# Kernel tuning notes

Measured on AMD Instinct MI355X. Metric: run time of the kernel, lower is better.

## Reference

```python
import jax, jax.numpy as jnp
import numpy as np

B, T, E, H, M = 1, 2048, 1536, 16, 3
KVH = 8
NREP = H // KVH
HD = E // H // M  # 32
EPS = 1e-5


def setup_inputs() -> dict:
    key = jax.random.key(0)
    ks = jax.random.split(key, 6)
    x = jax.random.normal(ks[0], (B, T, E), jnp.float32)
    # true rotary tables: freqs = pos * 10000^{-2i/d}, shape [T, HD//2]
    inv_freq = 1.0 / (10000.0 ** (np.arange(0, HD, 2, dtype=np.float64) / HD))
    ang = np.outer(np.arange(T, dtype=np.float64), inv_freq)
    cos = jnp.asarray(np.cos(ang), jnp.float32)
    sin = jnp.asarray(np.sin(ang), jnp.float32)
    s = 0.02
    q_w = s * jax.random.normal(ks[1], (M, E // M, E), jnp.float32)
    k_w = s * jax.random.normal(ks[2], (M, E // M // NREP, E), jnp.float32)
    v_w = s * jax.random.normal(ks[3], (E // NREP, E), jnp.float32)
    out_w = s * jax.random.normal(ks[4], (E, E), jnp.float32)
    raw_map_weights = jnp.array([0.1, -0.1, 0.1], jnp.float32)
    weight_scale = jnp.ones((1,), jnp.float32)
    subln_w = jnp.ones((M * HD,), jnp.float32)
    return dict(x=x, cos=cos, sin=sin, q_w=q_w, k_w=k_w, v_w=v_w,
                out_w=out_w, raw_map_weights=raw_map_weights,
                weight_scale=weight_scale, subln_w=subln_w)


def _rope_interleaved(t, cos, sin):
    # t: [..., seq, heads, hd]; cos/sin: [seq, hd//2]
    x1 = t[..., 0::2]
    x2 = t[..., 1::2]
    c = cos[:, None, :]
    s = sin[:, None, :]
    o1 = x1 * c - x2 * s
    o2 = x1 * s + x2 * c
    return jnp.stack([o1, o2], axis=-1).reshape(t.shape)


def reference(x, cos, sin, q_w, k_w, v_w, out_w, raw_map_weights, weight_scale, subln_w):
    b, t, e = x.shape
    m = q_w.shape[0]
    hd = 2 * cos.shape[-1]
    h = q_w.shape[1] // hd
    kvh = k_w.shape[1] // hd
    nrep = h // kvh
    scaling = hd ** -0.5

    map_w = jnp.tanh(raw_map_weights) * weight_scale  # [M]

    # per-map Q/K projections, all maps at once
    q = jnp.einsum('bte,mfe->mbtf', x, q_w).reshape(m, b, t, h, hd)
    k = jnp.einsum('bte,mfe->mbtf', x, k_w).reshape(m, b, t, kvh, hd)
    q = _rope_interleaved(q, cos, sin) * scaling
    k = _rope_interleaved(k, cos, sin)
    q = q.transpose(0, 1, 3, 2, 4)                      # [m,b,h,t,hd]
    k = jnp.repeat(k.transpose(0, 1, 3, 2, 4), nrep, axis=2)  # [m,b,h,t,hd]

    v = jnp.einsum('bte,fe->btf', x, v_w).reshape(b, t, kvh, m * hd)
    v = jnp.repeat(v.transpose(0, 2, 1, 3), nrep, axis=1)  # [b,h,t,m*hd]

    causal = jnp.where(jnp.triu(jnp.ones((t, t), bool), 1),
                       jnp.float32(-jnp.inf), jnp.float32(0.0))

    scores = jnp.einsum('mbhtd,mbhsd->mbhts', q, k)
    scores = jnp.nan_to_num(scores) + causal
    attn_w = jax.nn.softmax(scores.astype(jnp.float32), axis=-1).astype(x.dtype)
    combined = jnp.einsum('m,mbhts->bhts', map_w, attn_w)

    attn = jnp.einsum('bhts,bhsf->bhtf', combined, v)  # [b,h,t,m*hd]
    # RMSNorm over last dim
    var = jnp.mean(jnp.square(attn.astype(jnp.float32)), axis=-1, keepdims=True)
    attn = (attn * jax.lax.rsqrt(var + EPS)).astype(attn.dtype) * subln_w

    attn = attn.transpose(0, 2, 1, 3).reshape(b, t, h * m * hd)
    return jnp.einsum('bte,fe->btf', attn, out_w)
```

## Files before the change

### kernel.cpp

```cpp
#include <hip/hip_runtime.h>
#include <hip/hip_bf16.h>
#include <math.h>

#define T_DIM 2048
#define E_DIM 1536
#define K_DIM 1536

typedef unsigned short u16;
typedef unsigned int u32;
typedef __attribute__((ext_vector_type(8))) short bf16x8;
typedef __attribute__((ext_vector_type(4))) float f32x4;

__device__ __forceinline__ u16 f2bf(float x) {
    unsigned u = __float_as_uint(x);
    return (u16)((u + 0x7fffu + ((u >> 16) & 1u)) >> 16);
}

#define GLOAD16(gsrc, ldst)                                                              \
    __builtin_amdgcn_global_load_lds((const __attribute__((address_space(1))) u32*)(gsrc), \
                                     (__attribute__((address_space(3))) u32*)(ldst), 16, 0, 0)

__global__ __launch_bounds__(256) void cvt_bf16_5(const float* __restrict__ s0, u16* __restrict__ d0,
                                                  const float* __restrict__ s1, u16* __restrict__ d1,
                                                  const float* __restrict__ s2, u16* __restrict__ d2,
                                                  const float* __restrict__ s3, u16* __restrict__ d3,
                                                  const float* __restrict__ s4, u16* __restrict__ d4) {
    int i = blockIdx.x * 256 + threadIdx.x;
    const float* s;
    u16* d;
    int off;
    if (i < 786432)       { s = s0; d = d0; off = i; }
    else if (i < 1376256) { s = s1; d = d1; off = i - 786432; }
    else if (i < 1671168) { s = s2; d = d2; off = i - 1376256; }
    else if (i < 1966080) { s = s3; d = d3; off = i - 1671168; }
    else                  { s = s4; d = d4; off = i - 1966080; }
    float4 v = ((const float4*)s)[off];
    ((ushort4*)d)[off] = make_ushort4(f2bf(v.x), f2bf(v.y), f2bf(v.z), f2bf(v.w));
}

__global__ __launch_bounds__(256) void gemm_qkv_fused(const u16* __restrict__ A,
                                                      const u16* __restrict__ W,
                                                      const float* __restrict__ cosb,
                                                      const float* __restrict__ sinb,
                                                      u16* __restrict__ qb16,
                                                      u16* __restrict__ kpack,
                                                      u16* __restrict__ vpack,
                                                      float qscale) {
    const int K = K_DIM;
    __shared__ __align__(16) u16 As[128 * 64];
    __shared__ __align__(16) u16 Bs[128 * 64];
    const int tid = threadIdx.x;
    const int lane = tid & 63;
    const int wv = tid >> 6;
    const int wr = wv >> 1;
    const int wc = wv & 1;
    const int cl = lane & 15;
    const int g = lane >> 4;
    const int bm = blockIdx.y * 128;
    const int bn = blockIdx.x * 128;

    const char* Ab = (const char*)A;
    const char* Wb = (const char*)W;

    size_t a_src[4], b_src[4];
    int dst[4];
#pragma unroll
    for (int is = 0; is < 4; ++is) {
        int b = is * 4096 + tid * 16;
        int row = b >> 7;
        int wi = b & 127;
        dst[is] = b;
        a_src[is] = (size_t)(bm + row) * (K * 2) + (wi ^ ((row & 7) << 4));
        b_src[is] = (size_t)(bn + row) * (K * 2) + (wi ^ ((row & 7) << 4));
    }

    f32x4 acc[4][4];
#pragma unroll
    for (int mi = 0; mi < 4; ++mi)
#pragma unroll
        for (int ni = 0; ni < 4; ++ni) acc[mi][ni] = (f32x4){0.f, 0.f, 0.f, 0.f};

    for (int k0b = 0; k0b < K * 2; k0b += 128) {
#pragma unroll
        for (int is = 0; is < 4; ++is)
            GLOAD16(Ab + a_src[is] + k0b, (char*)As + dst[is]);
#pragma unroll
        for (int is = 0; is < 4; ++is)
            GLOAD16(Wb + b_src[is] + k0b, (char*)Bs + dst[is]);
        __syncthreads();
#pragma unroll
        for (int kk = 0; kk < 2; ++kk) {
            const int co = (kk * 64 + g * 16) ^ ((cl & 7) << 4);
            bf16x8 af[4], bfr[4];
#pragma unroll
            for (int mi = 0; mi < 4; ++mi)
                af[mi] = *(const bf16x8*)((const char*)As + (wr * 64 + mi * 16 + cl) * 128 + co);
#pragma unroll
            for (int ni = 0; ni < 4; ++ni)
                bfr[ni] = *(const bf16x8*)((const char*)Bs + (wc * 64 + ni * 16 + cl) * 128 + co);
#pragma unroll
            for (int mi = 0; mi < 4; ++mi)
#pragma unroll
                for (int ni = 0; ni < 4; ++ni)
                    acc[mi][ni] = __builtin_amdgcn_mfma_f32_16x16x32_bf16(af[mi], bfr[ni], acc[mi][ni], 0, 0, 0);
        }
        __syncthreads();
    }

    if (bn < 1536) {
#pragma unroll
        for (int mi = 0; mi < 4; ++mi)
#pragma unroll
            for (int ni = 0; ni < 4; ++ni)
#pragma unroll
                for (int r = 0; r < 4; ++r) {
                    int trow = bm + wr * 64 + mi * 16 + 4 * g + r;
                    int c = bn + wc * 64 + ni * 16 + cl;
                    float v = acc[mi][ni][r];
                    float pv = __shfl_xor(v, 1, 64);
                    int i = (c & 31) >> 1;
                    float cs = cosb[trow * 16 + i];
                    float sn = sinb[trow * 16 + i];
                    float o = v * cs + ((c & 1) ? pv * sn : -pv * sn);
                    qb16[(size_t)trow * E_DIM + c] = f2bf(o * qscale);
                }
    } else if (bn < 2304) {
#pragma unroll
        for (int mi = 0; mi < 4; ++mi)
#pragma unroll
            for (int ni = 0; ni < 4; ++ni)
#pragma unroll
                for (int r = 0; r < 4; ++r) {
                    int trow = bm + wr * 64 + mi * 16 + 4 * g + r;
                    int c = bn + wc * 64 + ni * 16 + cl;
                    float v = acc[mi][ni][r];
                    float pv = __shfl_xor(v, 1, 64);
                    int i = (c & 31) >> 1;
                    float cs = cosb[trow * 16 + i];
                    float sn = sinb[trow * 16 + i];
                    float o = v * cs + ((c & 1) ? pv * sn : -pv * sn);
                    int ck = c - 1536;
                    int m = ck >> 8;
                    int rem = ck & 255;
                    int kvhh = rem >> 5;
                    int d = rem & 31;
                    int cch = trow >> 5, st2 = (trow >> 4) & 1, colk = trow & 15;
                    size_t dstb = ((((size_t)(kvhh * 64 + cch) * 3 + m) * 2 + st2) * 16 + colk) * 32 + d;
                    kpack[dstb] = f2bf(o);
                }
    } else {
#pragma unroll
        for (int mi = 0; mi < 4; ++mi)
#pragma unroll
            for (int ni = 0; ni < 4; ++ni)
#pragma unroll
                for (int r = 0; r < 4; ++r) {
                    int trow = bm + wr * 64 + mi * 16 + 4 * g + r;
                    int c = bn + wc * 64 + ni * 16 + cl;
                    int fq = c - 2304;
                    int kvhh = fq / 96;
                    int f = fq - kvhh * 96;
                    size_t dstb = ((size_t)(kvhh * 64 + (trow >> 5)) * 96 + f) * 32 + (trow & 31);
                    vpack[dstb] = f2bf(acc[mi][ni][r]);
                }
    }
}

__global__ __launch_bounds__(256) void gemm_mfma_out(const u16* __restrict__ A,
                                                     const u16* __restrict__ W,
                                                     float* __restrict__ Cp,
                                                     int K, int ldC) {
    __shared__ __align__(16) u16 As[128 * 64];
    __shared__ __align__(16) u16 Bs[64 * 64];
    const int tid = threadIdx.x;
    const int lane = tid & 63;
    const int wv = tid >> 6;
    const int wr = wv >> 1;
    const int wc = wv & 1;
    const int cl = lane & 15;
    const int g = lane >> 4;
    const int bm = blockIdx.y * 128;
    const int bn = blockIdx.x * 64;

    const char* Ab = (const char*)A;
    const char* Wb = (const char*)W;

    size_t a_src[4];
    int a_dst[4];
#pragma unroll
    for (int is = 0; is < 4; ++is) {
        int b = is * 4096 + wv * 1024 + lane * 16;
        int row = b >> 7;
        int wi = b & 127;
        a_src[is] = (size_t)(bm + row) * (K * 2) + (wi ^ ((row & 7) << 4));
        a_dst[is] = b;
    }
    size_t b_src[2];
    int b_dst[2];
#pragma unroll
    for (int is = 0; is < 2; ++is) {
        int b = is * 4096 + wv * 1024 + lane * 16;
        int row = b >> 7;
        int wi = b & 127;
        b_src[is] = (size_t)(bn + row) * (K * 2) + (wi ^ ((row & 7) << 4));
        b_dst[is] = b;
    }

    f32x4 acc[4][2];
#pragma unroll
    for (int mi = 0; mi < 4; ++mi)
#pragma unroll
        for (int ni = 0; ni < 2; ++ni) acc[mi][ni] = (f32x4){0.f, 0.f, 0.f, 0.f};

    for (int k0b = 0; k0b < K * 2; k0b += 128) {
#pragma unroll
        for (int is = 0; is < 4; ++is)
            GLOAD16(Ab + a_src[is] + k0b, (char*)As + a_dst[is]);
#pragma unroll
        for (int is = 0; is < 2; ++is)
            GLOAD16(Wb + b_src[is] + k0b, (char*)Bs + b_dst[is]);
        __syncthreads();
#pragma unroll
        for (int kk = 0; kk < 2; ++kk) {
            const int co = (kk * 64 + g * 16) ^ ((cl & 7) << 4);
            bf16x8 af[4], bfr[2];
#pragma unroll
            for (int mi = 0; mi < 4; ++mi)
                af[mi] = *(const bf16x8*)((const char*)As + (wr * 64 + mi * 16 + cl) * 128 + co);
#pragma unroll
            for (int ni = 0; ni < 2; ++ni)
                bfr[ni] = *(const bf16x8*)((const char*)Bs + (wc * 32 + ni * 16 + cl) * 128 + co);
#pragma unroll
            for (int mi = 0; mi < 4; ++mi)
#pragma unroll
                for (int ni = 0; ni < 2; ++ni)
                    acc[mi][ni] = __builtin_amdgcn_mfma_f32_16x16x32_bf16(af[mi], bfr[ni], acc[mi][ni], 0, 0, 0);
        }
        __syncthreads();
    }

#pragma unroll
    for (int mi = 0; mi < 4; ++mi)
#pragma unroll
        for (int ni = 0; ni < 2; ++ni)
#pragma unroll
            for (int r = 0; r < 4; ++r) {
                size_t row = bm + wr * 64 + mi * 16 + 4 * g + r;
                size_t col = bn + wc * 32 + ni * 16 + cl;
                Cp[row * ldC + col] = acc[mi][ni][r];
            }
}

__global__ __launch_bounds__(256) void attn_fused(const u16* __restrict__ qb,
                                                  const u16* __restrict__ kpack,
                                                  const u16* __restrict__ vpack,
                                                  const float* __restrict__ raw_map,
                                                  const float* __restrict__ wscale,
                                                  const float* __restrict__ subln,
                                                  u16* __restrict__ outb) {
    __shared__ __align__(16) char smem[12288];
    const int tid = threadIdx.x;
    const int lane = tid & 63;
    const int wv = tid >> 6;
    const int col = lane & 15;
    const int g = lane >> 4;
    const int lid = blockIdx.x;
    const int kvh = lid & 7;
    const int rest = lid >> 3;
    const int h = kvh * 2 + (rest & 1);
    const int p = rest >> 1;

    u16 (*plds)[2][16][40] = (u16(*)[2][16][40])smem;
    float (*red2)[48] = (float(*)[48])smem;
    float (*red1)[3][2][16] = (float(*)[3][2][16])smem;

    float mw[3];
    {
        float wsc = wscale[0];
#pragma unroll
        for (int m = 0; m < 3; ++m) mw[m] = tanhf(raw_map[m]) * wsc;
    }
    const int laneoff = col * 32 + 8 * g;

    for (int half = 0; half < 2; ++half) {
        const int qt = half ? p : (63 - p);
        const int qbase = qt * 32;
        const int nfull = qt;

        bf16x8 qfrag[3][2];
#pragma unroll
        for (int m = 0; m < 3; ++m)
#pragma unroll
            for (int q2 = 0; q2 < 2; ++q2)
                qfrag[m][q2] = *(const bf16x8*)(qb + (size_t)(qbase + 16 * q2 + col) * E_DIM + m * 512 + h * 32 + 8 * g);

        float lsum[3][2] = {{0.f, 0.f}, {0.f, 0.f}, {0.f, 0.f}};
        {
            const u16* kt = kpack + (size_t)(kvh * 64 + wv) * 3072;
            for (int c = wv; c < nfull; c += 4) {
                bf16x8 kf[6];
#pragma unroll
                for (int u = 0; u < 6; ++u) kf[u] = *(const bf16x8*)(kt + laneoff + u * 512);
                kt += 4 * 3072;
                __builtin_amdgcn_s_setprio(1);
#pragma unroll
                for (int m = 0; m < 3; ++m)
#pragma unroll
                    for (int st = 0; st < 2; ++st)
#pragma unroll
                        for (int q2 = 0; q2 < 2; ++q2) {
                            f32x4 sv = __builtin_amdgcn_mfma_f32_16x16x32_bf16(
                                kf[m * 2 + st], qfrag[m][q2], (f32x4){0.f, 0.f, 0.f, 0.f}, 0, 0, 0);
                            lsum[m][q2] += (__builtin_amdgcn_exp2f(sv[0]) + __builtin_amdgcn_exp2f(sv[1])) +
                                           (__builtin_amdgcn_exp2f(sv[2]) + __builtin_amdgcn_exp2f(sv[3]));
                        }
                __builtin_amdgcn_s_setprio(0);
            }
            if ((nfull & 3) == wv) {
                const u16* ktm = kpack + (size_t)(kvh * 64 + nfull) * 3072 + laneoff;
                bf16x8 kf[6];
#pragma unroll
                for (int u = 0; u < 6; ++u) kf[u] = *(const bf16x8*)(ktm + u * 512);
#pragma unroll
                for (int m = 0; m < 3; ++m) {
                    {
                        f32x4 sv = __builtin_amdgcn_mfma_f32_16x16x32_bf16(
                            kf[m * 2 + 0], qfrag[m][0], (f32x4){0.f, 0.f, 0.f, 0.f}, 0, 0, 0);
#pragma unroll
                        for (int r = 0; r < 4; ++r) {
                            float x = (4 * g + r > col) ? -1e30f : sv[r];
                            lsum[m][0] += __builtin_amdgcn_exp2f(x);
                        }
                    }
                    {
                        f32x4 sv = __builtin_amdgcn_mfma_f32_16x16x32_bf16(
                            kf[m * 2 + 0], qfrag[m][1], (f32x4){0.f, 0.f, 0.f, 0.f}, 0, 0, 0);
                        lsum[m][1] += (__builtin_amdgcn_exp2f(sv[0]) + __builtin_amdgcn_exp2f(sv[1])) +
                                      (__builtin_amdgcn_exp2f(sv[2]) + __builtin_amdgcn_exp2f(sv[3]));
                    }
                    {
                        f32x4 sv = __builtin_amdgcn_mfma_f32_16x16x32_bf16(
                            kf[m * 2 + 1], qfrag[m][1], (f32x4){0.f, 0.f, 0.f, 0.f}, 0, 0, 0);
#pragma unroll
                        for (int r = 0; r < 4; ++r) {
                            float x = (4 * g + r > col) ? -1e30f : sv[r];
                            lsum[m][1] += __builtin_amdgcn_exp2f(x);
                        }
                    }
                }
            }
        }
#pragma unroll
        for (int m = 0; m < 3; ++m)
#pragma unroll
            for (int q2 = 0; q2 < 2; ++q2) {
                lsum[m][q2] += __shfl_xor(lsum[m][q2], 16, 64);
                lsum[m][q2] += __shfl_xor(lsum[m][q2], 32, 64);
            }
        if (g == 0) {
#pragma unroll
            for (int m = 0; m < 3; ++m)
#pragma unroll
                for (int q2 = 0; q2 < 2; ++q2) red1[wv][m][q2][col] = lsum[m][q2];
        }
        __syncthreads();
        float fac[3][2];
#pragma unroll
        for (int m = 0; m < 3; ++m)
#pragma unroll
            for (int q2 = 0; q2 < 2; ++q2)
                fac[m][q2] = mw[m] / (red1[0][m][q2][col] + red1[1][m][q2][col] +
                                      red1[2][m][q2][col] + red1[3][m][q2][col]);
        __syncthreads();

        f32x4 oacc[2][6];
#pragma unroll
        for (int q2 = 0; q2 < 2; ++q2)
#pragma unroll
            for (int ft = 0; ft < 6; ++ft) oacc[q2][ft] = (f32x4){0.f, 0.f, 0.f, 0.f};

        {
            const u16* kt = kpack + (size_t)(kvh * 64 + wv) * 3072;
            const u16* vt = vpack + (size_t)(kvh * 64 + wv) * 3072;
            for (int c = wv; c < nfull; c += 4) {
                bf16x8 kf[6], vf[6];
#pragma unroll
                for (int u = 0; u < 6; ++u) kf[u] = *(const bf16x8*)(kt + laneoff + u * 512);
#pragma unroll
                for (int u = 0; u < 6; ++u) vf[u] = *(const bf16x8*)(vt + laneoff + u * 512);
                kt += 4 * 3072;
                vt += 4 * 3072;

                __builtin_amdgcn_s_setprio(1);
#pragma unroll
                for (int q2 = 0; q2 < 2; ++q2)
#pragma unroll
                    for (int st = 0; st < 2; ++st) {
                        float pp[4] = {0.f, 0.f, 0.f, 0.f};
#pragma unroll
                        for (int m = 0; m < 3; ++m) {
                            f32x4 sv = __builtin_amdgcn_mfma_f32_16x16x32_bf16(
                                kf[m * 2 + st], qfrag[m][q2], (f32x4){0.f, 0.f, 0.f, 0.f}, 0, 0, 0);
#pragma unroll
                            for (int r = 0; r < 4; ++r)
                                pp[r] += fac[m][q2] * __builtin_amdgcn_exp2f(sv[r]);
                        }
                        __hip_bfloat162 b01 = __float22bfloat162_rn(make_float2(pp[0], pp[1]));
                        __hip_bfloat162 b23 = __float22bfloat162_rn(make_float2(pp[2], pp[3]));
                        uint2 w;
                        w.x = *(u32*)&b01;
                        w.y = *(u32*)&b23;
                        *(uint2*)&plds[wv][q2][col][st * 16 + 4 * g] = w;
                    }
#pragma unroll
                for (int q2 = 0; q2 < 2; ++q2) {
                    bf16x8 pf = *(const bf16x8*)&plds[wv][q2][col][8 * g];
#pragma unroll
                    for (int ft = 0; ft < 6; ++ft)
                        oacc[q2][ft] = __builtin_amdgcn_mfma_f32_16x16x32_bf16(pf, vf[ft], oacc[q2][ft], 0, 0, 0);
                }
                __builtin_amdgcn_s_setprio(0);
            }

            if ((nfull & 3) == wv) {
                const u16* ktm = kpack + (size_t)(kvh * 64 + nfull) * 3072 + laneoff;
                const u16* vtm = vpack + (size_t)(kvh * 64 + nfull) * 3072 + laneoff;
                bf16x8 kf[6], vf[6];
#pragma unroll
                for (int u = 0; u < 6; ++u) kf[u] = *(const bf16x8*)(ktm + u * 512);
#pragma unroll
                for (int u = 0; u < 6; ++u) vf[u] = *(const bf16x8*)(vtm + u * 512);

                {
                    float pp[4] = {0.f, 0.f, 0.f, 0.f};
#pragma unroll
                    for (int m = 0; m < 3; ++m) {
                        f32x4 sv = __builtin_amdgcn_mfma_f32_16x16x32_bf16(
                            kf[m * 2 + 0], qfrag[m][0], (f32x4){0.f, 0.f, 0.f, 0.f}, 0, 0, 0);
#pragma unroll
                        for (int r = 0; r < 4; ++r) {
                            float x = (4 * g + r > col) ? -1e30f : sv[r];
                            pp[r] += fac[m][0] * __builtin_amdgcn_exp2f(x);
                        }
                    }
                    __hip_bfloat162 b01 = __float22bfloat162_rn(make_float2(pp[0], pp[1]));
                    __hip_bfloat162 b23 = __float22bfloat162_rn(make_float2(pp[2], pp[3]));
                    uint2 w;
                    w.x = *(u32*)&b01;
                    w.y = *(u32*)&b23;
                    *(uint2*)&plds[wv][0][col][4 * g] = w;
                    uint2 z = make_uint2(0u, 0u);
                    *(uint2*)&plds[wv][0][col][16 + 4 * g] = z;
                }
                {
                    float p0[4] = {0.f, 0.f, 0.f, 0.f};
                    float p1[4] = {0.f, 0.f, 0.f, 0.f};
#pragma unroll
                    for (int m = 0; m < 3; ++m) {
                        f32x4 sv0 = __builtin_amdgcn_mfma_f32_16x16x32_bf16(
                            kf[m * 2 + 0], qfrag[m][1], (f32x4){0.f, 0.f, 0.f, 0.f}, 0, 0, 0);
                        f32x4 sv1 = __builtin_amdgcn_mfma_f32_16x16x32_bf16(
                            kf[m * 2 + 1], qfrag[m][1], (f32x4){0.f, 0.f, 0.f, 0.f}, 0, 0, 0);
#pragma unroll
                        for (int r = 0; r < 4; ++r) {
                            p0[r] += fac[m][1] * __builtin_amdgcn_exp2f(sv0[r]);
                            float x = (4 * g + r > col) ? -1e30f : sv1[r];
                            p1[r] += fac[m][1] * __builtin_amdgcn_exp2f(x);
                        }
                    }
                    __hip_bfloat162 a01 = __float22bfloat162_rn(make_float2(p0[0], p0[1]));
                    __hip_bfloat162 a23 = __float22bfloat162_rn(make_float2(p0[2], p0[3]));
                    uint2 w0;
                    w0.x = *(u32*)&a01;
                    w0.y = *(u32*)&a23;
                    *(uint2*)&plds[wv][1][col][4 * g] = w0;
                    __hip_bfloat162 b01 = __float22bfloat162_rn(make_float2(p1[0], p1[1]));
                    __hip_bfloat162 b23 = __float22bfloat162_rn(make_float2(p1[2], p1[3]));
                    uint2 w1;
                    w1.x = *(u32*)&b01;
                    w1.y = *(u32*)&b23;
                    *(uint2*)&plds[wv][1][col][16 + 4 * g] = w1;
                }
#pragma unroll
                for (int q2 = 0; q2 < 2; ++q2) {
                    bf16x8 pf = *(const bf16x8*)&plds[wv][q2][col][8 * g];
#pragma unroll
                    for (int ft = 0; ft < 6; ++ft)
                        oacc[q2][ft] = __builtin_amdgcn_mfma_f32_16x16x32_bf16(pf, vf[ft], oacc[q2][ft], 0, 0, 0);
                }
            }
        }

        __syncthreads();
#pragma unroll
        for (int src = 1; src < 4; ++src) {
            if (wv == src) {
                float4* rp = (float4*)red2[lane];
#pragma unroll
                for (int q2 = 0; q2 < 2; ++q2)
#pragma unroll
                    for (int ft = 0; ft < 6; ++ft)
                        rp[q2 * 6 + ft] = make_float4(oacc[q2][ft][0], oacc[q2][ft][1],
                                                      oacc[q2][ft][2], oacc[q2][ft][3]);
            }
            __syncthreads();
            if (wv == 0) {
                const float4* rp = (const float4*)red2[lane];
#pragma unroll
                for (int q2 = 0; q2 < 2; ++q2)
#pragma unroll
                    for (int ft = 0; ft < 6; ++ft) {
                        float4 a = rp[q2 * 6 + ft];
                        oacc[q2][ft][0] += a.x; oacc[q2][ft][1] += a.y;
                        oacc[q2][ft][2] += a.z; oacc[q2][ft][3] += a.w;
                    }
            }
            __syncthreads();
        }

        if (wv == 0) {
            float ss[2][4] = {{0.f, 0.f, 0.f, 0.f}, {0.f, 0.f, 0.f, 0.f}};
#pragma unroll
            for (int q2 = 0; q2 < 2; ++q2)
#pragma unroll
                for (int ft = 0; ft < 6; ++ft)
#pragma unroll
                    for (int r = 0; r < 4; ++r) ss[q2][r] += oacc[q2][ft][r] * oacc[q2][ft][r];
#pragma unroll
            for (int q2 = 0; q2 < 2; ++q2)
#pragma unroll
                for (int r = 0; r < 4; ++r) {
                    ss[q2][r] += __shfl_xor(ss[q2][r], 1, 64);
                    ss[q2][r] += __shfl_xor(ss[q2][r], 2, 64);
                    ss[q2][r] += __shfl_xor(ss[q2][r], 4, 64);
                    ss[q2][r] += __shfl_xor(ss[q2][r], 8, 64);
                    ss[q2][r] = rsqrtf(ss[q2][r] * (1.f / 96.f) + 1e-5f);
                }
#pragma unroll
            for (int ft = 0; ft < 6; ++ft) {
                float sl = subln[ft * 16 + col];
#pragma unroll
                for (int q2 = 0; q2 < 2; ++q2)
#pragma unroll
                    for (int r = 0; r < 4; ++r) {
                        int trow = qbase + 16 * q2 + 4 * g + r;
                        outb[(size_t)trow * E_DIM + h * 96 + ft * 16 + col] =
                            f2bf(oacc[q2][ft][r] * ss[q2][r] * sl);
                    }
            }
        }
        __syncthreads();
    }
}

extern "C" void kernel_launch(void* const* d_in, const int* in_sizes, int n_in,
                              void* d_out, int out_size, void* d_ws, size_t ws_size,
                              hipStream_t stream) {
    const float* x       = (const float*)d_in[0];
    const float* cosb    = (const float*)d_in[1];
    const float* sinb    = (const float*)d_in[2];
    const float* q_w     = (const float*)d_in[3];
    const float* k_w     = (const float*)d_in[4];
    const float* v_w     = (const float*)d_in[5];
    const float* out_w   = (const float*)d_in[6];
    const float* raw_map = (const float*)d_in[7];
    const float* wscale  = (const float*)d_in[8];
    const float* subln   = (const float*)d_in[9];
    float* out = (float*)d_out;

    char* ws = (char*)d_ws;
    u16* xb16   = (u16*)(ws);
    u16* wqkv16 = (u16*)(ws + 6291456);
    u16* qb16   = (u16*)(ws + 15728640);
    u16* kpack  = (u16*)(ws + 22020096);
    u16* vpack  = (u16*)(ws + 25190400);
    u16* wout16 = (u16*)(ws + 28360704);
    u16* ab16   = xb16;

    cvt_bf16_5<<<9984, 256, 0, stream>>>(x, xb16,
                                         q_w, wqkv16,
                                         k_w, wqkv16 + 2359296,
                                         v_w, wqkv16 + 3538944,
                                         out_w, wout16);

    const float qscale = 0.17677669529663687f * 1.4426950408889634f;
    gemm_qkv_fused<<<dim3(3072 / 128, T_DIM / 128), 256, 0, stream>>>(
        xb16, wqkv16, cosb, sinb, qb16, kpack, vpack, qscale);

    attn_fused<<<512, 256, 0, stream>>>(qb16, kpack, vpack, raw_map, wscale, subln, ab16);

    gemm_mfma_out<<<dim3(E_DIM / 64, T_DIM / 128), 256, 0, stream>>>(ab16, wout16, out, K_DIM, E_DIM);
}
```

Measured before the change: 127.4 us.

## Use eight waves per attention block with a tree reduction of partial outputs

Doubles the attention kernel's block size from four to eight waves, so each block splits its causal key tiles across eight waves instead of four. The cross-wave reduction of the partial output accumulators becomes a three-level tree over a larger shared-memory buffer, replacing the sequential one-wave-at-a-time reduction. The aim is to raise per-block parallelism and latency hiding on a grid of only 512 blocks. The cost is more shared memory per block and added reduction and synchronisation overhead, and the launch-bounds change may limit registers per thread.

Result: slower. 311.0 us (+144.2%).

```diff
diff --git a/kernel.cpp b/kernel.cpp
--- a/kernel.cpp
+++ b/kernel.cpp
@@ -251,14 +251,14 @@
             }
 }
 
-__global__ __launch_bounds__(256) void attn_fused(const u16* __restrict__ qb,
-                                                  const u16* __restrict__ kpack,
-                                                  const u16* __restrict__ vpack,
-                                                  const float* __restrict__ raw_map,
-                                                  const float* __restrict__ wscale,
-                                                  const float* __restrict__ subln,
-                                                  u16* __restrict__ outb) {
-    __shared__ __align__(16) char smem[12288];
+__global__ __launch_bounds__(512, 4) void attn_fused(const u16* __restrict__ qb,
+                                                     const u16* __restrict__ kpack,
+                                                     const u16* __restrict__ vpack,
+                                                     const float* __restrict__ raw_map,
+                                                     const float* __restrict__ wscale,
+                                                     const float* __restrict__ subln,
+                                                     u16* __restrict__ outb) {
+    __shared__ __align__(16) char smem[49152];
     const int tid = threadIdx.x;
     const int lane = tid & 63;
     const int wv = tid >> 6;
@@ -271,8 +271,8 @@
     const int p = rest >> 1;
 
     u16 (*plds)[2][16][40] = (u16(*)[2][16][40])smem;
-    float (*red2)[48] = (float(*)[48])smem;
     float (*red1)[3][2][16] = (float(*)[3][2][16])smem;
+    float* redA = (float*)smem;
 
     float mw[3];
     {
@@ -297,11 +297,11 @@
         float lsum[3][2] = {{0.f, 0.f}, {0.f, 0.f}, {0.f, 0.f}};
         {
             const u16* kt = kpack + (size_t)(kvh * 64 + wv) * 3072;
-            for (int c = wv; c < nfull; c += 4) {
+            for (int c = wv; c < nfull; c += 8) {
                 bf16x8 kf[6];
 #pragma unroll
                 for (int u = 0; u < 6; ++u) kf[u] = *(const bf16x8*)(kt + laneoff + u * 512);
-                kt += 4 * 3072;
+                kt += 8 * 3072;
                 __builtin_amdgcn_s_setprio(1);
 #pragma unroll
                 for (int m = 0; m < 3; ++m)
@@ -316,7 +316,7 @@
                         }
                 __builtin_amdgcn_s_setprio(0);
             }
-            if ((nfull & 3) == wv) {
+            if ((nfull & 7) == wv) {
                 const u16* ktm = kpack + (size_t)(kvh * 64 + nfull) * 3072 + laneoff;
                 bf16x8 kf[6];
 #pragma unroll
@@ -368,9 +368,12 @@
 #pragma unroll
         for (int m = 0; m < 3; ++m)
 #pragma unroll
-            for (int q2 = 0; q2 < 2; ++q2)
-                fac[m][q2] = mw[m] / (red1[0][m][q2][col] + red1[1][m][q2][col] +
-                                      red1[2][m][q2][col] + red1[3][m][q2][col]);
+            for (int q2 = 0; q2 < 2; ++q2) {
+                float tot = 0.f;
+#pragma unroll
+                for (int w8 = 0; w8 < 8; ++w8) tot += red1[w8][m][q2][col];
+                fac[m][q2] = mw[m] / tot;
+            }
         __syncthreads();
 
         f32x4 oacc[2][6];
@@ -382,14 +385,14 @@
         {
             const u16* kt = kpack + (size_t)(kvh * 64 + wv) * 3072;
             const u16* vt = vpack + (size_t)(kvh * 64 + wv) * 3072;
-            for (int c = wv; c < nfull; c += 4) {
+            for (int c = wv; c < nfull; c += 8) {
                 bf16x8 kf[6], vf[6];
 #pragma unroll
                 for (int u = 0; u < 6; ++u) kf[u] = *(const bf16x8*)(kt + laneoff + u * 512);
 #pragma unroll
                 for (int u = 0; u < 6; ++u) vf[u] = *(const bf16x8*)(vt + laneoff + u * 512);
-                kt += 4 * 3072;
-                vt += 4 * 3072;
+                kt += 8 * 3072;
+                vt += 8 * 3072;
 
                 __builtin_amdgcn_s_setprio(1);
 #pragma unroll
@@ -422,7 +425,7 @@
                 __builtin_amdgcn_s_setprio(0);
             }
 
-            if ((nfull & 3) == wv) {
+            if ((nfull & 7) == wv) {
                 const u16* ktm = kpack + (size_t)(kvh * 64 + nfull) * 3072 + laneoff;
                 const u16* vtm = vpack + (size_t)(kvh * 64 + nfull) * 3072 + laneoff;
                 bf16x8 kf[6], vf[6];
@@ -492,33 +495,71 @@
         }
 
         __syncthreads();
-#pragma unroll
-        for (int src = 1; src < 4; ++src) {
-            if (wv == src) {
-                float4* rp = (float4*)red2[lane];
-#pragma unroll
-                for (int q2 = 0; q2 < 2; ++q2)
-#pragma unroll
-                    for (int ft = 0; ft < 6; ++ft)
-                        rp[q2 * 6 + ft] = make_float4(oacc[q2][ft][0], oacc[q2][ft][1],
-                                                      oacc[q2][ft][2], oacc[q2][ft][3]);
-            }
-            __syncthreads();
-            if (wv == 0) {
-                const float4* rp = (const float4*)red2[lane];
-#pragma unroll
-                for (int q2 = 0; q2 < 2; ++q2)
-#pragma unroll
-                    for (int ft = 0; ft < 6; ++ft) {
-                        float4 a = rp[q2 * 6 + ft];
-                        oacc[q2][ft][0] += a.x; oacc[q2][ft][1] += a.y;
-                        oacc[q2][ft][2] += a.z; oacc[q2][ft][3] += a.w;
-                    }
-            }
-            __syncthreads();
-        }
-
+        if (wv >= 4) {
+            float4* rp = (float4*)(redA + ((size_t)(wv - 4) * 64 + lane) * 48);
+#pragma unroll
+            for (int q2 = 0; q2 < 2; ++q2)
+#pragma unroll
+                for (int ft = 0; ft < 6; ++ft)
+                    rp[q2 * 6 + ft] = make_float4(oacc[q2][ft][0], oacc[q2][ft][1],
+                                                  oacc[q2][ft][2], oacc[q2][ft][3]);
+        }
+        __syncthreads();
+        if (wv < 4) {
+            const float4* rp = (const float4*)(redA + ((size_t)wv * 64 + lane) * 48);
+#pragma unroll
+            for (int q2 = 0; q2 < 2; ++q2)
+#pragma unroll
+                for (int ft = 0; ft < 6; ++ft) {
+                    float4 a = rp[q2 * 6 + ft];
+                    oacc[q2][ft][0] += a.x; oacc[q2][ft][1] += a.y;
+                    oacc[q2][ft][2] += a.z; oacc[q2][ft][3] += a.w;
+                }
+        }
+        __syncthreads();
+        if (wv == 2 || wv == 3) {
+            float4* rp = (float4*)(redA + ((size_t)(wv - 2) * 64 + lane) * 48);
+#pragma unroll
+            for (int q2 = 0; q2 < 2; ++q2)
+#pragma unroll
+                for (int ft = 0; ft < 6; ++ft)
+                    rp[q2 * 6 + ft] = make_float4(oacc[q2][ft][0], oacc[q2][ft][1],
+                                                  oacc[q2][ft][2], oacc[q2][ft][3]);
+        }
+        __syncthreads();
+        if (wv < 2) {
+            const float4* rp = (const float4*)(redA + ((size_t)wv * 64 + lane) * 48);
+#pragma unroll
+            for (int q2 = 0; q2 < 2; ++q2)
+#pragma unroll
+                for (int ft = 0; ft < 6; ++ft) {
+                    float4 a = rp[q2 * 6 + ft];
+                    oacc[q2][ft][0] += a.x; oacc[q2][ft][1] += a.y;
+                    oacc[q2][ft][2] += a.z; oacc[q2][ft][3] += a.w;
+                }
+        }
+        __syncthreads();
+        if (wv == 1) {
+            float4* rp = (float4*)(redA + (size_t)lane * 48);
+#pragma unroll
+            for (int q2 = 0; q2 < 2; ++q2)
+#pragma unroll
+                for (int ft = 0; ft < 6; ++ft)
+                    rp[q2 * 6 + ft] = make_float4(oacc[q2][ft][0], oacc[q2][ft][1],
+                                                  oacc[q2][ft][2], oacc[q2][ft][3]);
+        }
+        __syncthreads();
         if (wv == 0) {
+            const float4* rp = (const float4*)(redA + (size_t)lane * 48);
+#pragma unroll
+            for (int q2 = 0; q2 < 2; ++q2)
+#pragma unroll
+                for (int ft = 0; ft < 6; ++ft) {
+                    float4 a = rp[q2 * 6 + ft];
+                    oacc[q2][ft][0] += a.x; oacc[q2][ft][1] += a.y;
+                    oacc[q2][ft][2] += a.z; oacc[q2][ft][3] += a.w;
+                }
+
             float ss[2][4] = {{0.f, 0.f, 0.f, 0.f}, {0.f, 0.f, 0.f, 0.f}};
 #pragma unroll
             for (int q2 = 0; q2 < 2; ++q2)
@@ -587,7 +628,7 @@
     gemm_qkv_fused<<<dim3(3072 / 128, T_DIM / 128), 256, 0, stream>>>(
         xb16, wqkv16, cosb, sinb, qb16, kpack, vpack, qscale);
 
-    attn_fused<<<512, 256, 0, stream>>>(qb16, kpack, vpack, raw_map, wscale, subln, ab16);
+    attn_fused<<<512, 512, 0, stream>>>(qb16, kpack, vpack, raw_map, wscale, subln, ab16);
 
     gemm_mfma_out<<<dim3(E_DIM / 64, T_DIM / 128), 256, 0, stream>>>(ab16, wout16, out, K_DIM, E_DIM);
 }
```

## Fuse softmax sum and PV into one pass with post-normalization per map

Applied to the files above, without the earlier changes.

Replaces the two-pass attention kernel with a single-pass kernel. It accumulates unnormalized exp(QK)·V separately per map, then scales each map's partial output by map_weight/row_sum before summing across maps. This removes the separate row-sum pass, which recomputed every QK MFMA and exp. The work is also regrouped: 6 waves per block (3 maps × 2 key-strided waves), one 32-row query tile per block with heavy tiles launched first, instead of each block pairing a light and a heavy tile. The cost is a larger LDS reduction across 6 waves and extra bf16 rounding of unnormalized probabilities.

After: 133.7 us. +5.0%, slower.

```diff
diff --git a/kernel.cpp b/kernel.cpp
--- a/kernel.cpp
+++ b/kernel.cpp
@@ -251,305 +251,245 @@
             }
 }
 
-__global__ __launch_bounds__(256) void attn_fused(const u16* __restrict__ qb,
-                                                  const u16* __restrict__ kpack,
-                                                  const u16* __restrict__ vpack,
-                                                  const float* __restrict__ raw_map,
-                                                  const float* __restrict__ wscale,
-                                                  const float* __restrict__ subln,
-                                                  u16* __restrict__ outb) {
-    __shared__ __align__(16) char smem[12288];
+__global__ __launch_bounds__(384) void attn_one(const u16* __restrict__ qb,
+                                                const u16* __restrict__ kpack,
+                                                const u16* __restrict__ vpack,
+                                                const float* __restrict__ raw_map,
+                                                const float* __restrict__ wscale,
+                                                const float* __restrict__ subln,
+                                                u16* __restrict__ outb) {
+    __shared__ __align__(16) char smem[36864];
     const int tid = threadIdx.x;
     const int lane = tid & 63;
     const int wv = tid >> 6;
+    const int m = wv >> 1;
+    const int ks = wv & 1;
     const int col = lane & 15;
     const int g = lane >> 4;
-    const int lid = blockIdx.x;
+    const int lid = blockIdx.y * 64 + blockIdx.x;
     const int kvh = lid & 7;
     const int rest = lid >> 3;
     const int h = kvh * 2 + (rest & 1);
-    const int p = rest >> 1;
-
-    u16 (*plds)[2][16][40] = (u16(*)[2][16][40])smem;
-    float (*red2)[48] = (float(*)[48])smem;
-    float (*red1)[3][2][16] = (float(*)[3][2][16])smem;
-
-    float mw[3];
+    const int qt = 63 - (rest >> 1);
+    const int qbase = qt * 32;
+    const int nfull = qt;
+
+    u16 (*plds)[2][16][48] = (u16(*)[2][16][48])smem;
+    float (*red1)[2][16] = (float(*)[2][16])smem;
+
+    bf16x8 qfrag[2];
+#pragma unroll
+    for (int q2 = 0; q2 < 2; ++q2)
+        qfrag[q2] = *(const bf16x8*)(qb + (size_t)(qbase + 16 * q2 + col) * E_DIM + m * 512 + h * 32 + 8 * g);
+
+    f32x4 oacc[2][6];
+#pragma unroll
+    for (int q2 = 0; q2 < 2; ++q2)
+#pragma unroll
+        for (int ft = 0; ft < 6; ++ft) oacc[q2][ft] = (f32x4){0.f, 0.f, 0.f, 0.f};
+    float lsum[2] = {0.f, 0.f};
+
+    const int laneoff = col * 32 + 8 * g;
+    const u16* kt = kpack + ((size_t)(kvh * 64 + ks) * 3 + m) * 1024 + laneoff;
+    const u16* vt = vpack + (size_t)(kvh * 64 + ks) * 3072 + laneoff;
+
+    for (int c = ks; c < nfull; c += 2) {
+        bf16x8 kf0 = *(const bf16x8*)(kt);
+        bf16x8 kf1 = *(const bf16x8*)(kt + 512);
+        bf16x8 vf[6];
+#pragma unroll
+        for (int u = 0; u < 6; ++u) vf[u] = *(const bf16x8*)(vt + u * 512);
+        kt += 2 * 3072;
+        vt += 2 * 3072;
+
+        __builtin_amdgcn_s_setprio(1);
+#pragma unroll
+        for (int q2 = 0; q2 < 2; ++q2) {
+            f32x4 sv0 = __builtin_amdgcn_mfma_f32_16x16x32_bf16(kf0, qfrag[q2], (f32x4){0.f, 0.f, 0.f, 0.f}, 0, 0, 0);
+            f32x4 sv1 = __builtin_amdgcn_mfma_f32_16x16x32_bf16(kf1, qfrag[q2], (f32x4){0.f, 0.f, 0.f, 0.f}, 0, 0, 0);
+            float p0 = __builtin_amdgcn_exp2f(sv0[0]);
+            float p1 = __builtin_amdgcn_exp2f(sv0[1]);
+            float p2 = __builtin_amdgcn_exp2f(sv0[2]);
+            float p3 = __builtin_amdgcn_exp2f(sv0[3]);
+            float p4 = __builtin_amdgcn_exp2f(sv1[0]);
+            float p5 = __builtin_amdgcn_exp2f(sv1[1]);
+            float p6 = __builtin_amdgcn_exp2f(sv1[2]);
+            float p7 = __builtin_amdgcn_exp2f(sv1[3]);
+            lsum[q2] += ((p0 + p1) + (p2 + p3)) + ((p4 + p5) + (p6 + p7));
+            __hip_bfloat162 a01 = __float22bfloat162_rn(make_float2(p0, p1));
+            __hip_bfloat162 a23 = __float22bfloat162_rn(make_float2(p2, p3));
+            __hip_bfloat162 b01 = __float22bfloat162_rn(make_float2(p4, p5));
+            __hip_bfloat162 b23 = __float22bfloat162_rn(make_float2(p6, p7));
+            uint2 w0, w1;
+            w0.x = *(u32*)&a01; w0.y = *(u32*)&a23;
+            w1.x = *(u32*)&b01; w1.y = *(u32*)&b23;
+            *(uint2*)&plds[wv][q2][col][4 * g] = w0;
+            *(uint2*)&plds[wv][q2][col][16 + 4 * g] = w1;
+        }
+#pragma unroll
+        for (int q2 = 0; q2 < 2; ++q2) {
+            bf16x8 pf = *(const bf16x8*)&plds[wv][q2][col][8 * g];
+#pragma unroll
+            for (int ft = 0; ft < 6; ++ft)
+                oacc[q2][ft] = __builtin_amdgcn_mfma_f32_16x16x32_bf16(pf, vf[ft], oacc[q2][ft], 0, 0, 0);
+        }
+        __builtin_amdgcn_s_setprio(0);
+    }
+
+    if ((nfull & 1) == ks) {
+        const u16* ktm = kpack + ((size_t)(kvh * 64 + nfull) * 3 + m) * 1024 + laneoff;
+        const u16* vtm = vpack + (size_t)(kvh * 64 + nfull) * 3072 + laneoff;
+        bf16x8 kf0 = *(const bf16x8*)(ktm);
+        bf16x8 kf1 = *(const bf16x8*)(ktm + 512);
+        bf16x8 vf[6];
+#pragma unroll
+        for (int u = 0; u < 6; ++u) vf[u] = *(const bf16x8*)(vtm + u * 512);
+
+        {
+            f32x4 sv = __builtin_amdgcn_mfma_f32_16x16x32_bf16(kf0, qfrag[0], (f32x4){0.f, 0.f, 0.f, 0.f}, 0, 0, 0);
+            float p[4];
+#pragma unroll
+            for (int r = 0; r < 4; ++r) {
+                float x = (4 * g + r > col) ? -1e30f : sv[r];
+                p[r] = __builtin_amdgcn_exp2f(x);
+                lsum[0] += p[r];
+            }
+            __hip_bfloat162 a01 = __float22bfloat162_rn(make_float2(p[0], p[1]));
+            __hip_bfloat162 a23 = __float22bfloat162_rn(make_float2(p[2], p[3]));
+            uint2 w0;
+            w0.x = *(u32*)&a01; w0.y = *(u32*)&a23;
+            *(uint2*)&plds[wv][0][col][4 * g] = w0;
+            uint2 z = make_uint2(0u, 0u);
+            *(uint2*)&plds[wv][0][col][16 + 4 * g] = z;
+        }
+        {
+            f32x4 sv0 = __builtin_amdgcn_mfma_f32_16x16x32_bf16(kf0, qfrag[1], (f32x4){0.f, 0.f, 0.f, 0.f}, 0, 0, 0);
+            f32x4 sv1 = __builtin_amdgcn_mfma_f32_16x16x32_bf16(kf1, qfrag[1], (f32x4){0.f, 0.f, 0.f, 0.f}, 0, 0, 0);
+            float p0[4], p1[4];
+#pragma unroll
+            for (int r = 0; r < 4; ++r) {
+                p0[r] = __builtin_amdgcn_exp2f(sv0[r]);
+                float x = (4 * g + r > col) ? -1e30f : sv1[r];
+                p1[r] = __builtin_amdgcn_exp2f(x);
+                lsum[1] += p0[r] + p1[r];
+            }
+            __hip_bfloat162 a01 = __float22bfloat162_rn(make_float2(p0[0], p0[1]));
+            __hip_bfloat162 a23 = __float22bfloat162_rn(make_float2(p0[2], p0[3]));
+            __hip_bfloat162 b01 = __float22bfloat162_rn(make_float2(p1[0], p1[1]));
+            __hip_bfloat162 b23 = __float22bfloat162_rn(make_float2(p1[2], p1[3]));
+            uint2 w0, w1;
+            w0.x = *(u32*)&a01; w0.y = *(u32*)&a23;
+            w1.x = *(u32*)&b01; w1.y = *(u32*)&b23;
+            *(uint2*)&plds[wv][1][col][4 * g] = w0;
+            *(uint2*)&plds[wv][1][col][16 + 4 * g] = w1;
+        }
+#pragma unroll
+        for (int q2 = 0; q2 < 2; ++q2) {
+            bf16x8 pf = *(const bf16x8*)&plds[wv][q2][col][8 * g];
+#pragma unroll
+            for (int ft = 0; ft < 6; ++ft)
+                oacc[q2][ft] = __builtin_amdgcn_mfma_f32_16x16x32_bf16(pf, vf[ft], oacc[q2][ft], 0, 0, 0);
+        }
+    }
+
+#pragma unroll
+    for (int q2 = 0; q2 < 2; ++q2) {
+        lsum[q2] += __shfl_xor(lsum[q2], 16, 64);
+        lsum[q2] += __shfl_xor(lsum[q2], 32, 64);
+    }
+    __syncthreads();
+    if (g == 0) {
+#pragma unroll
+        for (int q2 = 0; q2 < 2; ++q2) red1[wv][q2][col] = lsum[q2];
+    }
+    __syncthreads();
+
     {
-        float wsc = wscale[0];
-#pragma unroll
-        for (int m = 0; m < 3; ++m) mw[m] = tanhf(raw_map[m]) * wsc;
-    }
-    const int laneoff = col * 32 + 8 * g;
-
-    for (int half = 0; half < 2; ++half) {
-        const int qt = half ? p : (63 - p);
-        const int qbase = qt * 32;
-        const int nfull = qt;
-
-        bf16x8 qfrag[3][2];
-#pragma unroll
-        for (int m = 0; m < 3; ++m)
-#pragma unroll
-            for (int q2 = 0; q2 < 2; ++q2)
-                qfrag[m][q2] = *(const bf16x8*)(qb + (size_t)(qbase + 16 * q2 + col) * E_DIM + m * 512 + h * 32 + 8 * g);
-
-        float lsum[3][2] = {{0.f, 0.f}, {0.f, 0.f}, {0.f, 0.f}};
-        {
-            const u16* kt = kpack + (size_t)(kvh * 64 + wv) * 3072;
-            for (int c = wv; c < nfull; c += 4) {
-                bf16x8 kf[6];
-#pragma unroll
-                for (int u = 0; u < 6; ++u) kf[u] = *(const bf16x8*)(kt + laneoff + u * 512);
-                kt += 4 * 3072;
-                __builtin_amdgcn_s_setprio(1);
-#pragma unroll
-                for (int m = 0; m < 3; ++m)
-#pragma unroll
-                    for (int st = 0; st < 2; ++st)
-#pragma unroll
-                        for (int q2 = 0; q2 < 2; ++q2) {
-                            f32x4 sv = __builtin_amdgcn_mfma_f32_16x16x32_bf16(
-                                kf[m * 2 + st], qfrag[m][q2], (f32x4){0.f, 0.f, 0.f, 0.f}, 0, 0, 0);
-                            lsum[m][q2] += (__builtin_amdgcn_exp2f(sv[0]) + __builtin_amdgcn_exp2f(sv[1])) +
-                                           (__builtin_amdgcn_exp2f(sv[2]) + __builtin_amdgcn_exp2f(sv[3]));
-                        }
-                __builtin_amdgcn_s_setprio(0);
-            }
-            if ((nfull & 3) == wv) {
-                const u16* ktm = kpack + (size_t)(kvh * 64 + nfull) * 3072 + laneoff;
-                bf16x8 kf[6];
-#pragma unroll
-                for (int u = 0; u < 6; ++u) kf[u] = *(const bf16x8*)(ktm + u * 512);
-#pragma unroll
-                for (int m = 0; m < 3; ++m) {
-                    {
-                        f32x4 sv = __builtin_amdgcn_mfma_f32_16x16x32_bf16(
-                            kf[m * 2 + 0], qfrag[m][0], (f32x4){0.f, 0.f, 0.f, 0.f}, 0, 0, 0);
-#pragma unroll
-                        for (int r = 0; r < 4; ++r) {
-                            float x = (4 * g + r > col) ? -1e30f : sv[r];
-                            lsum[m][0] += __builtin_amdgcn_exp2f(x);
-                        }
-                    }
-                    {
-                        f32x4 sv = __builtin_amdgcn_mfma_f32_16x16x32_bf16(
-                            kf[m * 2 + 0], qfrag[m][1], (f32x4){0.f, 0.f, 0.f, 0.f}, 0, 0, 0);
-                        lsum[m][1] += (__builtin_amdgcn_exp2f(sv[0]) + __builtin_amdgcn_exp2f(sv[1])) +
-                                      (__builtin_amdgcn_exp2f(sv[2]) + __builtin_amdgcn_exp2f(sv[3]));
-                    }
-                    {
-                        f32x4 sv = __builtin_amdgcn_mfma_f32_16x16x32_bf16(
-                            kf[m * 2 + 1], qfrag[m][1], (f32x4){0.f, 0.f, 0.f, 0.f}, 0, 0, 0);
-#pragma unroll
-                        for (int r = 0; r < 4; ++r) {
-                            float x = (4 * g + r > col) ? -1e30f : sv[r];
-                            lsum[m][1] += __builtin_amdgcn_exp2f(x);
-                        }
-                    }
-                }
-            }
-        }
-#pragma unroll
-        for (int m = 0; m < 3; ++m)
-#pragma unroll
-            for (int q2 = 0; q2 < 2; ++q2) {
-                lsum[m][q2] += __shfl_xor(lsum[m][q2], 16, 64);
-                lsum[m][q2] += __shfl_xor(lsum[m][q2], 32, 64);
-            }
-        if (g == 0) {
-#pragma unroll
-            for (int m = 0; m < 3; ++m)
-#pragma unroll
-                for (int q2 = 0; q2 < 2; ++q2) red1[wv][m][q2][col] = lsum[m][q2];
-        }
-        __syncthreads();
-        float fac[3][2];
-#pragma unroll
-        for (int m = 0; m < 3; ++m)
-#pragma unroll
-            for (int q2 = 0; q2 < 2; ++q2)
-                fac[m][q2] = mw[m] / (red1[0][m][q2][col] + red1[1][m][q2][col] +
-                                      red1[2][m][q2][col] + red1[3][m][q2][col]);
-        __syncthreads();
-
-        f32x4 oacc[2][6];
+        float mwm = tanhf(raw_map[m]) * wscale[0];
 #pragma unroll
         for (int q2 = 0; q2 < 2; ++q2)
 #pragma unroll
-            for (int ft = 0; ft < 6; ++ft) oacc[q2][ft] = (f32x4){0.f, 0.f, 0.f, 0.f};
-
-        {
-            const u16* kt = kpack + (size_t)(kvh * 64 + wv) * 3072;
-            const u16* vt = vpack + (size_t)(kvh * 64 + wv) * 3072;
-            for (int c = wv; c < nfull; c += 4) {
-                bf16x8 kf[6], vf[6];
-#pragma unroll
-                for (int u = 0; u < 6; ++u) kf[u] = *(const bf16x8*)(kt + laneoff + u * 512);
-#pragma unroll
-                for (int u = 0; u < 6; ++u) vf[u] = *(const bf16x8*)(vt + laneoff + u * 512);
-                kt += 4 * 3072;
-                vt += 4 * 3072;
-
-                __builtin_amdgcn_s_setprio(1);
-#pragma unroll
-                for (int q2 = 0; q2 < 2; ++q2)
-#pragma unroll
-                    for (int st = 0; st < 2; ++st) {
-                        float pp[4] = {0.f, 0.f, 0.f, 0.f};
-#pragma unroll
-                        for (int m = 0; m < 3; ++m) {
-                            f32x4 sv = __builtin_amdgcn_mfma_f32_16x16x32_bf16(
-                                kf[m * 2 + st], qfrag[m][q2], (f32x4){0.f, 0.f, 0.f, 0.f}, 0, 0, 0);
-#pragma unroll
-                            for (int r = 0; r < 4; ++r)
-                                pp[r] += fac[m][q2] * __builtin_amdgcn_exp2f(sv[r]);
-                        }
-                        __hip_bfloat162 b01 = __float22bfloat162_rn(make_float2(pp[0], pp[1]));
-                        __hip_bfloat162 b23 = __float22bfloat162_rn(make_float2(pp[2], pp[3]));
-                        uint2 w;
-                        w.x = *(u32*)&b01;
-                        w.y = *(u32*)&b23;
-                        *(uint2*)&plds[wv][q2][col][st * 16 + 4 * g] = w;
-                    }
-#pragma unroll
-                for (int q2 = 0; q2 < 2; ++q2) {
-                    bf16x8 pf = *(const bf16x8*)&plds[wv][q2][col][8 * g];
-#pragma unroll
-                    for (int ft = 0; ft < 6; ++ft)
-                        oacc[q2][ft] = __builtin_amdgcn_mfma_f32_16x16x32_bf16(pf, vf[ft], oacc[q2][ft], 0, 0, 0);
-                }
-                __builtin_amdgcn_s_setprio(0);
-            }
-
-            if ((nfull & 3) == wv) {
-                const u16* ktm = kpack + (size_t)(kvh * 64 + nfull) * 3072 + laneoff;
-                const u16* vtm = vpack + (size_t)(kvh * 64 + nfull) * 3072 + laneoff;
-                bf16x8 kf[6], vf[6];
-#pragma unroll
-                for (int u = 0; u < 6; ++u) kf[u] = *(const bf16x8*)(ktm + u * 512);
-#pragma unroll
-                for (int u = 0; u < 6; ++u) vf[u] = *(const bf16x8*)(vtm + u * 512);
-
-                {
-                    float pp[4] = {0.f, 0.f, 0.f, 0.f};
-#pragma unroll
-                    for (int m = 0; m < 3; ++m) {
-                        f32x4 sv = __builtin_amdgcn_mfma_f32_16x16x32_bf16(
-                            kf[m * 2 + 0], qfrag[m][0], (f32x4){0.f, 0.f, 0.f, 0.f}, 0, 0, 0);
-#pragma unroll
-                        for (int r = 0; r < 4; ++r) {
-                            float x = (4 * g + r > col) ? -1e30f : sv[r];
-                            pp[r] += fac[m][0] * __builtin_amdgcn_exp2f(x);
-                        }
-                    }
-                    __hip_bfloat162 b01 = __float22bfloat162_rn(make_float2(pp[0], pp[1]));
-                    __hip_bfloat162 b23 = __float22bfloat162_rn(make_float2(pp[2], pp[3]));
-                    uint2 w;
-                    w.x = *(u32*)&b01;
-                    w.y = *(u32*)&b23;
-                    *(uint2*)&plds[wv][0][col][4 * g] = w;
-                    uint2 z = make_uint2(0u, 0u);
-                    *(uint2*)&plds[wv][0][col][16 + 4 * g] = z;
-                }
-                {
-                    float p0[4] = {0.f, 0.f, 0.f, 0.f};
-                    float p1[4] = {0.f, 0.f, 0.f, 0.f};
-#pragma unroll
-                    for (int m = 0; m < 3; ++m) {
-                        f32x4 sv0 = __builtin_amdgcn_mfma_f32_16x16x32_bf16(
-                            kf[m * 2 + 0], qfrag[m][1], (f32x4){0.f, 0.f, 0.f, 0.f}, 0, 0, 0);
-                        f32x4 sv1 = __builtin_amdgcn_mfma_f32_16x16x32_bf16(
-                            kf[m * 2 + 1], qfrag[m][1], (f32x4){0.f, 0.f, 0.f, 0.f}, 0, 0, 0);
-#pragma unroll
-                        for (int r = 0; r < 4; ++r) {
-                            p0[r] += fac[m][1] * __builtin_amdgcn_exp2f(sv0[r]);
-                            float x = (4 * g + r > col) ? -1e30f : sv1[r];
-                            p1[r] += fac[m][1] * __builtin_amdgcn_exp2f(x);
-                        }
-                    }
-                    __hip_bfloat162 a01 = __float22bfloat162_rn(make_float2(p0[0], p0[1]));
-                    __hip_bfloat162 a23 = __float22bfloat162_rn(make_float2(p0[2], p0[3]));
-                    uint2 w0;
-                    w0.x = *(u32*)&a01;
-                    w0.y = *(u32*)&a23;
-                    *(uint2*)&plds[wv][1][col][4 * g] = w0;
-                    __hip_bfloat162 b01 = __float22bfloat162_rn(make_float2(p1[0], p1[1]));
-                    __hip_bfloat162 b23 = __float22bfloat162_rn(make_float2(p1[2], p1[3]));
-                    uint2 w1;
-                    w1.x = *(u32*)&b01;
-                    w1.y = *(u32*)&b23;
-                    *(uint2*)&plds[wv][1][col][16 + 4 * g] = w1;
-                }
-#pragma unroll
-                for (int q2 = 0; q2 < 2; ++q2) {
-                    bf16x8 pf = *(const bf16x8*)&plds[wv][q2][col][8 * g];
-#pragma unroll
-                    for (int ft = 0; ft < 6; ++ft)
-                        oacc[q2][ft] = __builtin_amdgcn_mfma_f32_16x16x32_bf16(pf, vf[ft], oacc[q2][ft], 0, 0, 0);
-                }
-            }
-        }
-
-        __syncthreads();
-#pragma unroll
-        for (int src = 1; src < 4; ++src) {
-            if (wv == src) {
-                float4* rp = (float4*)red2[lane];
-#pragma unroll
-                for (int q2 = 0; q2 < 2; ++q2)
-#pragma unroll
-                    for (int ft = 0; ft < 6; ++ft)
-                        rp[q2 * 6 + ft] = make_float4(oacc[q2][ft][0], oacc[q2][ft][1],
-                                                      oacc[q2][ft][2], oacc[q2][ft][3]);
-            }
-            __syncthreads();
-            if (wv == 0) {
-                const float4* rp = (const float4*)red2[lane];
-#pragma unroll
-                for (int q2 = 0; q2 < 2; ++q2)
-#pragma unroll
-                    for (int ft = 0; ft < 6; ++ft) {
-                        float4 a = rp[q2 * 6 + ft];
-                        oacc[q2][ft][0] += a.x; oacc[q2][ft][1] += a.y;
-                        oacc[q2][ft][2] += a.z; oacc[q2][ft][3] += a.w;
-                    }
-            }
-            __syncthreads();
-        }
-
-        if (wv == 0) {
-            float ss[2][4] = {{0.f, 0.f, 0.f, 0.f}, {0.f, 0.f, 0.f, 0.f}};
-#pragma unroll
-            for (int q2 = 0; q2 < 2; ++q2)
-#pragma unroll
-                for (int ft = 0; ft < 6; ++ft)
-#pragma unroll
-                    for (int r = 0; r < 4; ++r) ss[q2][r] += oacc[q2][ft][r] * oacc[q2][ft][r];
-#pragma unroll
-            for (int q2 = 0; q2 < 2; ++q2)
-#pragma unroll
-                for (int r = 0; r < 4; ++r) {
-                    ss[q2][r] += __shfl_xor(ss[q2][r], 1, 64);
-                    ss[q2][r] += __shfl_xor(ss[q2][r], 2, 64);
-                    ss[q2][r] += __shfl_xor(ss[q2][r], 4, 64);
-                    ss[q2][r] += __shfl_xor(ss[q2][r], 8, 64);
-                    ss[q2][r] = rsqrtf(ss[q2][r] * (1.f / 96.f) + 1e-5f);
-                }
+            for (int r = 0; r < 4; ++r) {
+                float tot = red1[2 * m][q2][4 * g + r] + red1[2 * m + 1][q2][4 * g + r];
+                float f = mwm / tot;
+                oacc[q2][0][r] *= f; oacc[q2][1][r] *= f; oacc[q2][2][r] *= f;
+                oacc[q2][3][r] *= f; oacc[q2][4][r] *= f; oacc[q2][5][r] *= f;
+            }
+    }
+    __syncthreads();
+
+    float* redA = (float*)smem;
+    if (wv >= 3) {
+        float4* rp = (float4*)(redA + (size_t)(wv - 3) * 3072 + (size_t)lane * 48);
+#pragma unroll
+        for (int q2 = 0; q2 < 2; ++q2)
+#pragma unroll
+            for (int ft = 0; ft < 6; ++ft)
+                rp[q2 * 6 + ft] = make_float4(oacc[q2][ft][0], oacc[q2][ft][1], oacc[q2][ft][2], oacc[q2][ft][3]);
+    }
+    __syncthreads();
+    if (wv < 3) {
+        const float4* rp = (const float4*)(redA + (size_t)wv * 3072 + (size_t)lane * 48);
+#pragma unroll
+        for (int q2 = 0; q2 < 2; ++q2)
 #pragma unroll
             for (int ft = 0; ft < 6; ++ft) {
-                float sl = subln[ft * 16 + col];
-#pragma unroll
-                for (int q2 = 0; q2 < 2; ++q2)
-#pragma unroll
-                    for (int r = 0; r < 4; ++r) {
-                        int trow = qbase + 16 * q2 + 4 * g + r;
-                        outb[(size_t)trow * E_DIM + h * 96 + ft * 16 + col] =
-                            f2bf(oacc[q2][ft][r] * ss[q2][r] * sl);
-                    }
-            }
-        }
-        __syncthreads();
+                float4 a = rp[q2 * 6 + ft];
+                oacc[q2][ft][0] += a.x; oacc[q2][ft][1] += a.y;
+                oacc[q2][ft][2] += a.z; oacc[q2][ft][3] += a.w;
+            }
+    }
+    __syncthreads();
+    if (wv == 1 || wv == 2) {
+        float4* rp = (float4*)(redA + (size_t)(wv - 1) * 3072 + (size_t)lane * 48);
+#pragma unroll
+        for (int q2 = 0; q2 < 2; ++q2)
+#pragma unroll
+            for (int ft = 0; ft < 6; ++ft)
+                rp[q2 * 6 + ft] = make_float4(oacc[q2][ft][0], oacc[q2][ft][1], oacc[q2][ft][2], oacc[q2][ft][3]);
+    }
+    __syncthreads();
+    if (wv != 0) return;
+#pragma unroll
+    for (int s2 = 0; s2 < 2; ++s2) {
+        const float4* rp = (const float4*)(redA + (size_t)s2 * 3072 + (size_t)lane * 48);
+#pragma unroll
+        for (int q2 = 0; q2 < 2; ++q2)
+#pragma unroll
+            for (int ft = 0; ft < 6; ++ft) {
+                float4 a = rp[q2 * 6 + ft];
+                oacc[q2][ft][0] += a.x; oacc[q2][ft][1] += a.y;
+                oacc[q2][ft][2] += a.z; oacc[q2][ft][3] += a.w;
+            }
+    }
+
+    float ss[2][4] = {{0.f, 0.f, 0.f, 0.f}, {0.f, 0.f, 0.f, 0.f}};
+#pragma unroll
+    for (int q2 = 0; q2 < 2; ++q2)
+#pragma unroll
+        for (int ft = 0; ft < 6; ++ft)
+#pragma unroll
+            for (int r = 0; r < 4; ++r) ss[q2][r] += oacc[q2][ft][r] * oacc[q2][ft][r];
+#pragma unroll
+    for (int q2 = 0; q2 < 2; ++q2)
+#pragma unroll
+        for (int r = 0; r < 4; ++r) {
+            ss[q2][r] += __shfl_xor(ss[q2][r], 1, 64);
+            ss[q2][r] += __shfl_xor(ss[q2][r], 2, 64);
+            ss[q2][r] += __shfl_xor(ss[q2][r], 4, 64);
+            ss[q2][r] += __shfl_xor(ss[q2][r], 8, 64);
+            ss[q2][r] = rsqrtf(ss[q2][r] * (1.f / 96.f) + 1e-5f);
+        }
+#pragma unroll
+    for (int ft = 0; ft < 6; ++ft) {
+        float sl = subln[ft * 16 + col];
+#pragma unroll
+        for (int q2 = 0; q2 < 2; ++q2)
+#pragma unroll
+            for (int r = 0; r < 4; ++r) {
+                int trow = qbase + 16 * q2 + 4 * g + r;
+                outb[(size_t)trow * E_DIM + h * 96 + ft * 16 + col] = f2bf(oacc[q2][ft][r] * ss[q2][r] * sl);
+            }
     }
 }
 
@@ -587,7 +527,7 @@
     gemm_qkv_fused<<<dim3(3072 / 128, T_DIM / 128), 256, 0, stream>>>(
         xb16, wqkv16, cosb, sinb, qb16, kpack, vpack, qscale);
 
-    attn_fused<<<512, 256, 0, stream>>>(qb16, kpack, vpack, raw_map, wscale, subln, ab16);
+    attn_one<<<dim3(64, 16), 384, 0, stream>>>(qb16, kpack, vpack, raw_map, wscale, subln, ab16);
 
     gemm_mfma_out<<<dim3(E_DIM / 64, T_DIM / 128), 256, 0, stream>>>(ab16, wout16, out, K_DIM, E_DIM);
 }
```
